# Performance work log

Hardware: AMD Instinct MI355X
Metric: run time of the kernel (lower is better)

## Reference

```python
import jax, jax.numpy as jnp
import numpy as np

BETA = 0.25
EPS = 1e-12

def normalise(x):
    # L2 normalise over last axis
    return x / jnp.sqrt(jnp.sum(x * x, axis=-1, keepdims=True) + EPS)

def setup_inputs() -> dict:
    key = jax.random.key(0)
    k = jax.random.split(key, 6)
    N, d, c, P = 8192, 768, 256, 16384
    return {
        "z": jax.random.normal(k[0], (N, d), dtype=jnp.float32),
        "W_in": jax.random.normal(k[1], (d, c), dtype=jnp.float32) * 0.02,
        "b_in": jnp.zeros((c,), dtype=jnp.float32),
        "W_out": jax.random.normal(k[2], (c, d), dtype=jnp.float32) * 0.02,
        "b_out": jnp.zeros((d,), dtype=jnp.float32),
        "codebook": jax.random.normal(k[3], (P, c), dtype=jnp.float32),
    }

def reference(z, W_in, b_in, W_out, b_out, codebook):
    sg = jax.lax.stop_gradient
    # input projection + L2 normalise
    zq = normalise(z @ W_in + b_in)                 # [N, c]
    cb = normalise(codebook)                        # [P, c]
    # squared euclidean distances: ||z||^2 - 2 z.c + ||c||^2
    dist = (jnp.sum(zq * zq, axis=-1, keepdims=True)
            - 2.0 * jnp.einsum('nc,pc->np', zq, cb)
            + jnp.sum(cb * cb, axis=-1)[None, :])   # [N, P]
    idxes = jnp.argmin(dist, axis=-1)               # [N]
    codes = normalise(codebook[idxes])              # gather + normalise, [N, c]
    loss = BETA * (zq - sg(codes)) ** 2 + (sg(zq) - codes) ** 2
    # straight-through estimator
    codes = zq + sg(codes - zq)
    out = codes @ W_out + b_out                     # [N, d]
    return out, loss, idxes
```

## Files before the change

### kernel.cpp

```cpp
#include <hip/hip_runtime.h>
#include <hip/hip_fp16.h>
#include <math.h>

#define NN 8192
#define DD 768
#define CC 256
#define PP 16384
#define NG 256
#define MARGIN 5.0e-3f
#define BETA_C 1.25f
#define EPS_C 1e-12f

typedef __attribute__((ext_vector_type(8))) _Float16 f16x8;
typedef __attribute__((ext_vector_type(8))) short bf16x8;
typedef __attribute__((ext_vector_type(4))) float f32x4;
typedef __attribute__((ext_vector_type(16))) float f32x16;

static __device__ __forceinline__ ushort f2h(float x) {
    _Float16 h = (_Float16)x;
    return __builtin_bit_cast(unsigned short, h);
}
static __device__ __forceinline__ ushort f2bf(float x) {
    unsigned u = __float_as_uint(x);
    return (ushort)((u + 0x7fffu + ((u >> 16) & 1u)) >> 16);
}
static __device__ __forceinline__ float bf2f(ushort h) {
    return __uint_as_float(((unsigned)h) << 16);
}

static __device__ __forceinline__ void gload_lds16(const void* g, void* l) {
    __builtin_amdgcn_global_load_lds(
        (const __attribute__((address_space(1))) unsigned int*)g,
        (__attribute__((address_space(3))) unsigned int*)l, 16, 0, 0);
}

__global__ __launch_bounds__(256) void k_gemm_in(const float* __restrict__ z,
    const float* __restrict__ W, const float* __restrict__ b,
    float* __restrict__ zq)
{
    __shared__ float zt[64][36];
    __shared__ float wt[32][68];
    const int t = threadIdx.x;
    const int ti = t >> 4, tj = t & 15;
    const int n0 = blockIdx.x * 64;
    const int c0 = blockIdx.y * 64;

    f32x4 acc[4];
#pragma unroll
    for (int r = 0; r < 4; ++r) acc[r] = (f32x4){0.f, 0.f, 0.f, 0.f};

    for (int k0 = 0; k0 < DD; k0 += 32) {
        __syncthreads();
#pragma unroll
        for (int l = 0; l < 2; ++l) {
            int idx = l * 256 + t;
            int row = idx >> 3, c4 = idx & 7;
            *reinterpret_cast<float4*>(&zt[row][c4 * 4]) =
                *reinterpret_cast<const float4*>(&z[(size_t)(n0 + row) * DD + k0 + c4 * 4]);
            int krow = idx >> 4, w4 = idx & 15;
            *reinterpret_cast<float4*>(&wt[krow][w4 * 4]) =
                *reinterpret_cast<const float4*>(&W[(size_t)(k0 + krow) * CC + c0 + w4 * 4]);
        }
        __syncthreads();
#pragma unroll
        for (int kk = 0; kk < 32; kk += 4) {
            float4 a4[4], b4[4];
#pragma unroll
            for (int r = 0; r < 4; ++r)
                a4[r] = *reinterpret_cast<const float4*>(&zt[ti * 4 + r][kk]);
#pragma unroll
            for (int q = 0; q < 4; ++q)
                b4[q] = *reinterpret_cast<const float4*>(&wt[kk + q][tj * 4]);
#pragma unroll
            for (int q = 0; q < 4; ++q)
#pragma unroll
                for (int r = 0; r < 4; ++r) {
                    float av = ((const float*)&a4[r])[q];
                    acc[r].x += av * b4[q].x;
                    acc[r].y += av * b4[q].y;
                    acc[r].z += av * b4[q].z;
                    acc[r].w += av * b4[q].w;
                }
        }
    }
#pragma unroll
    for (int r = 0; r < 4; ++r) {
        int col = c0 + tj * 4;
        float4 o;
        o.x = acc[r].x + b[col];
        o.y = acc[r].y + b[col + 1];
        o.z = acc[r].z + b[col + 2];
        o.w = acc[r].w + b[col + 3];
        *reinterpret_cast<float4*>(&zq[(size_t)(n0 + ti * 4 + r) * CC + col]) = o;
    }
}

__global__ __launch_bounds__(256) void k_norm2(const float* __restrict__ src,
    float* __restrict__ dstf32, ushort* __restrict__ dsth,
    float* __restrict__ sq, float* __restrict__ rinvout, int rows)
{
    const int wave = threadIdx.x >> 6;
    const int lane = threadIdx.x & 63;
    const int row = blockIdx.x * 4 + wave;
    if (row >= rows) return;
    float4 v = *reinterpret_cast<const float4*>(&src[(size_t)row * CC + lane * 4]);
    float s = v.x * v.x + v.y * v.y + v.z * v.z + v.w * v.w;
#pragma unroll
    for (int off = 32; off; off >>= 1) s += __shfl_xor(s, off, 64);
    float r = 1.0f / sqrtf(s + EPS_C);
    v.x *= r; v.y *= r; v.z *= r; v.w *= r;
    if (dstf32)
        *reinterpret_cast<float4*>(&dstf32[(size_t)row * CC + lane * 4]) = v;
    ushort4 hv;
    hv.x = f2h(v.x); hv.y = f2h(v.y); hv.z = f2h(v.z); hv.w = f2h(v.w);
    *reinterpret_cast<ushort4*>(&dsth[(size_t)row * CC + lane * 4]) = hv;
    if (sq) {
        float s2 = v.x * v.x + v.y * v.y + v.z * v.z + v.w * v.w;
#pragma unroll
        for (int off = 32; off; off >>= 1) s2 += __shfl_xor(s2, off, 64);
        if (lane == 0) {
            sq[row] = s2;
            if (rinvout) rinvout[row] = r;
        }
    }
}

__global__ __launch_bounds__(256) void k_split_w(const float* __restrict__ W,
    ushort* __restrict__ wthi, ushort* __restrict__ wtlo)
{
    __shared__ float tile[64][68];
    const int t = threadIdx.x;
    const int d0 = blockIdx.x * 64;
    const int k0 = blockIdx.y * 64;
#pragma unroll
    for (int i = 0; i < 16; ++i) {
        int row = i * 4 + (t >> 6);
        int col = t & 63;
        tile[row][col] = W[(size_t)(k0 + row) * DD + d0 + col];
    }
    __syncthreads();
#pragma unroll
    for (int i = 0; i < 16; ++i) {
        int drow = i * 4 + (t >> 6);
        int kc = t & 63;
        float v = tile[kc][drow];
        ushort hi = f2bf(v);
        float rres = v - bf2f(hi);
        ushort lo = f2bf(rres);
        wthi[(size_t)(d0 + drow) * CC + k0 + kc] = hi;
        wtlo[(size_t)(d0 + drow) * CC + k0 + kc] = lo;
    }
}

__global__ __launch_bounds__(512) void k_dist(
    const ushort* __restrict__ cbh, const ushort* __restrict__ zqh,
    const float* __restrict__ cz2,
    float* __restrict__ gmin, unsigned long long* __restrict__ maskA)
{
    __shared__ ushort lds[2][16384];
    const int t = threadIdx.x;
    const int lane = t & 63;
    const int w = t >> 6;
    const int wr = w >> 2;
    const int wc = w & 3;

    const int id = blockIdx.x;
    const int l = (id & 7) * 256 + (id >> 3);
    const int p0 = (l & 63) * 256;
    const int n0 = (l >> 6) * 256;

    const int kh = lane >> 5;
    const int r31 = lane & 31;

    f32x16 acc[4][2];
#pragma unroll
    for (int mi = 0; mi < 4; ++mi) {
        const int pbm = p0 + wr * 128 + mi * 32;
#pragma unroll
        for (int q = 0; q < 4; ++q) {
            float4 cz = *reinterpret_cast<const float4*>(&cz2[pbm + q * 8 + kh * 4]);
#pragma unroll
            for (int j = 0; j < 4; ++j) {
                float v = -0.5f * ((const float*)&cz.x)[j];
                acc[mi][0][q * 4 + j] = v;
                acc[mi][1][q * 4 + j] = v;
            }
        }
    }

    const int u_l = lane >> 3;
    const int e = (lane & 7) ^ u_l;
    const int hh = e >> 2, jj = e & 3;
    const ushort* srcA[2];
    const ushort* srcB[2];
#pragma unroll
    for (int i = 0; i < 2; ++i)
        srcA[i] = cbh + (size_t)(p0 + 2 * (w * 16 + i * 8 + u_l) + hh) * CC + jj * 8;
#pragma unroll
    for (int i = 0; i < 2; ++i)
        srcB[i] = zqh + (size_t)(n0 + 2 * (w * 16 + i * 8 + u_l) + hh) * CC + jj * 8;

#define STAGE(BUF, KT)                                                        \
    {                                                                         \
        _Pragma("unroll")                                                     \
        for (int i = 0; i < 2; ++i)                                           \
            gload_lds16(srcA[i] + (KT) * 32, &lds[BUF][(w * 16 + i * 8) * 64]); \
        _Pragma("unroll")                                                     \
        for (int i = 0; i < 2; ++i)                                           \
            gload_lds16(srcB[i] + (KT) * 32, &lds[BUF][8192 + (w * 16 + i * 8) * 64]); \
    }

    const int ua = wr * 64 + (r31 >> 1);
    const int ub = wc * 32 + (r31 >> 1);
    const int hb = (r31 & 1) * 4 + kh;

#define COMPUTE(BUF)                                                          \
    {                                                                         \
        _Pragma("unroll")                                                     \
        for (int ks = 0; ks < 2; ++ks) {                                      \
            f16x8 af[4], bfv[2];                                              \
            _Pragma("unroll")                                                 \
            for (int mi = 0; mi < 4; ++mi) {                                  \
                int u = ua + mi * 16;                                         \
                af[mi] = *reinterpret_cast<const f16x8*>(                     \
                    &lds[BUF][u * 64 + (((hb + ks * 2) ^ (u & 7)) * 8)]);     \
            }                                                                 \
            _Pragma("unroll")                                                 \
            for (int ni = 0; ni < 2; ++ni) {                                  \
                int u = ub + ni * 16;                                         \
                bfv[ni] = *reinterpret_cast<const f16x8*>(                    \
                    &lds[BUF][8192 + u * 64 + (((hb + ks * 2) ^ (u & 7)) * 8)]); \
            }                                                                 \
            __builtin_amdgcn_s_setprio(1);                                    \
            acc[0][0] = __builtin_amdgcn_mfma_f32_32x32x16_f16(af[0], bfv[0], acc[0][0], 0, 0, 0); \
            acc[0][1] = __builtin_amdgcn_mfma_f32_32x32x16_f16(af[0], bfv[1], acc[0][1], 0, 0, 0); \
            acc[1][0] = __builtin_amdgcn_mfma_f32_32x32x16_f16(af[1], bfv[0], acc[1][0], 0, 0, 0); \
            acc[1][1] = __builtin_amdgcn_mfma_f32_32x32x16_f16(af[1], bfv[1], acc[1][1], 0, 0, 0); \
            acc[2][0] = __builtin_amdgcn_mfma_f32_32x32x16_f16(af[2], bfv[0], acc[2][0], 0, 0, 0); \
            acc[2][1] = __builtin_amdgcn_mfma_f32_32x32x16_f16(af[2], bfv[1], acc[2][1], 0, 0, 0); \
            acc[3][0] = __builtin_amdgcn_mfma_f32_32x32x16_f16(af[3], bfv[0], acc[3][0], 0, 0, 0); \
            acc[3][1] = __builtin_amdgcn_mfma_f32_32x32x16_f16(af[3], bfv[1], acc[3][1], 0, 0, 0); \
            __builtin_amdgcn_s_setprio(0);                                    \
        }                                                                     \
    }

#define BODY(KT, VM, DOSTAGE)                                                 \
    {                                                                         \
        if (DOSTAGE) STAGE(((KT) + 1) & 1, (KT) + 1);                         \
        __builtin_amdgcn_sched_barrier(0);                                    \
        asm volatile("s_waitcnt vmcnt(" #VM ")" ::: "memory");                \
        __builtin_amdgcn_s_barrier();                                         \
        __builtin_amdgcn_sched_barrier(0);                                    \
        COMPUTE((KT) & 1);                                                    \
        if ((KT) < 7) __builtin_amdgcn_s_barrier();                           \
    }

    STAGE(0, 0);
    BODY(0, 4, 1)
    BODY(1, 4, 1)
    BODY(2, 4, 1)
    BODY(3, 4, 1)
    BODY(4, 4, 1)
    BODY(5, 4, 1)
    BODY(6, 4, 1)
    BODY(7, 0, 0)

#undef BODY
#undef COMPUTE
#undef STAGE

#pragma unroll
    for (int ni = 0; ni < 2; ++ni) {
#pragma unroll
        for (int g = 0; g < 2; ++g) {
            float M = -1e30f;
#pragma unroll
            for (int m2 = 0; m2 < 2; ++m2)
#pragma unroll
                for (int r = 0; r < 16; ++r) M = fmaxf(M, acc[g * 2 + m2][ni][r]);
            M = fmaxf(M, __shfl_xor(M, 32, 64));
            const float thr = M - 0.5f * MARGIN;
            unsigned long long msk = 0ull;
#pragma unroll
            for (int m2 = 0; m2 < 2; ++m2)
#pragma unroll
                for (int q = 0; q < 4; ++q) {
                    unsigned nib = 0u;
#pragma unroll
                    for (int j = 0; j < 4; ++j)
                        nib |= (acc[g * 2 + m2][ni][q * 4 + j] >= thr) ? (1u << j) : 0u;
                    msk |= (unsigned long long)nib << (m2 * 32 + q * 8 + kh * 4);
                }
            msk |= __shfl_xor(msk, 32, 64);
            if (kh == 0) {
                int n = n0 + wc * 64 + ni * 32 + r31;
                int grp = (p0 >> 6) + wr * 2 + g;
                gmin[(size_t)n * NG + grp] = -2.0f * M;
                maskA[(size_t)n * NG + grp] = msk;
            }
        }
    }
}

__global__ __launch_bounds__(256) void k_pick(
    const float* __restrict__ gmin, const unsigned long long* __restrict__ maskA,
    const float* __restrict__ zqn, const float* __restrict__ cb_raw,
    const float* __restrict__ rinv, const float* __restrict__ cz2,
    float* __restrict__ idxf, ushort* __restrict__ chi,
    ushort* __restrict__ clo, float* __restrict__ loss)
{
    __shared__ int lst[4][256];
    __shared__ int cnt[4];
    const int t = threadIdx.x;
    const int w = t >> 6;
    const int lane = t & 63;
    const int row = blockIdx.x * 4 + w;

    float4 zr = *reinterpret_cast<const float4*>(&zqn[(size_t)row * CC + lane * 4]);
    float4 gv = *reinterpret_cast<const float4*>(&gmin[(size_t)row * NG + lane * 4]);

    float pm = fminf(fminf(gv.x, gv.y), fminf(gv.z, gv.w));
#pragma unroll
    for (int off = 1; off < 64; off <<= 1) pm = fminf(pm, __shfl_xor(pm, off, 64));
    const float thresh = pm + MARGIN;

    if (lane == 0) cnt[w] = 0;
    __syncthreads();
    {
        const float g4[4] = {gv.x, gv.y, gv.z, gv.w};
#pragma unroll
        for (int j = 0; j < 4; ++j)
            if (g4[j] <= thresh) {
                int pos = atomicAdd(&cnt[w], 1);
                lst[w][pos] = lane * 4 + j;
            }
    }
    __syncthreads();

    const int nc = cnt[w];
    unsigned long long best = ~0ull;
    for (int ci = 0; ci < nc; ++ci) {
        int g = lst[w][ci];
        unsigned long long msk = maskA[(size_t)row * NG + g];
        while (msk) {
            int bit = __ffsll((long long)msk) - 1;
            msk &= msk - 1;
            int p = g * 64 + bit;
            float rv = rinv[p];
            float4 c4 = *reinterpret_cast<const float4*>(&cb_raw[(size_t)p * CC + lane * 4]);
            float part = (c4.x * rv) * zr.x + (c4.y * rv) * zr.y
                       + (c4.z * rv) * zr.z + (c4.w * rv) * zr.w;
#pragma unroll
            for (int off = 1; off < 64; off <<= 1) part += __shfl_xor(part, off, 64);
            float d4 = fmaf(-2.0f, part, 4.0f + cz2[p]);
            unsigned long long pk = ((unsigned long long)__float_as_uint(d4) << 32) | (unsigned)p;
            best = best < pk ? best : pk;
        }
    }
    const int p = (int)(best & 0xffffffffu);
    if (lane == 0) idxf[row] = (float)p;

    const float rv = rinv[p];
    float4 cv = *reinterpret_cast<const float4*>(&cb_raw[(size_t)p * CC + lane * 4]);
    cv.x *= rv; cv.y *= rv; cv.z *= rv; cv.w *= rv;
    ushort4 hv, lv16;
    hv.x = f2bf(cv.x); lv16.x = f2bf(cv.x - bf2f(hv.x));
    hv.y = f2bf(cv.y); lv16.y = f2bf(cv.y - bf2f(hv.y));
    hv.z = f2bf(cv.z); lv16.z = f2bf(cv.z - bf2f(hv.z));
    hv.w = f2bf(cv.w); lv16.w = f2bf(cv.w - bf2f(hv.w));
    *reinterpret_cast<ushort4*>(&chi[(size_t)row * CC + lane * 4]) = hv;
    *reinterpret_cast<ushort4*>(&clo[(size_t)row * CC + lane * 4]) = lv16;
    float4 lsv;
    float dx = zr.x - cv.x, dy = zr.y - cv.y, dz = zr.z - cv.z, dw = zr.w - cv.w;
    lsv.x = BETA_C * dx * dx; lsv.y = BETA_C * dy * dy;
    lsv.z = BETA_C * dz * dz; lsv.w = BETA_C * dw * dw;
    *reinterpret_cast<float4*>(&loss[(size_t)row * CC + lane * 4]) = lsv;
}

__global__ __launch_bounds__(256) void k_gemm_out_mfma(
    const ushort* __restrict__ chi, const ushort* __restrict__ clo,
    const ushort* __restrict__ wthi, const ushort* __restrict__ wtlo,
    const float* __restrict__ bout, float* __restrict__ out)
{
    __shared__ ushort sAh[128 * 64];
    __shared__ ushort sAl[128 * 64];
    __shared__ ushort sBh[128 * 64];
    __shared__ ushort sBl[128 * 64];
    const int t = threadIdx.x;
    const int lane = t & 63;
    const int w = t >> 6;
    const int wr = w >> 1;
    const int wc = w & 1;
    const int nb = blockIdx.x * 128;
    const int db = blockIdx.y * 128;
    const int kh = lane >> 5;
    const int r31 = lane & 31;

    f32x16 acc[2][2];
#pragma unroll
    for (int mi = 0; mi < 2; ++mi)
#pragma unroll
        for (int ni = 0; ni < 2; ++ni)
#pragma unroll
            for (int r = 0; r < 16; ++r) acc[mi][ni][r] = 0.f;

    const int srow = lane >> 3;
    const int schunk = (lane & 7) ^ srow;
    const size_t rowA = (size_t)(nb + w * 32 + srow) * CC;
    const size_t rowB = (size_t)(db + w * 32 + srow) * CC;
    const char* sAhsrc = (const char*)chi + rowA * 2 + schunk * 16;
    const char* sAlsrc = (const char*)clo + rowA * 2 + schunk * 16;
    const char* sBhsrc = (const char*)wthi + rowB * 2 + schunk * 16;
    const char* sBlsrc = (const char*)wtlo + rowB * 2 + schunk * 16;
    char* dA = (char*)sAh + (w * 32) * 128;
    char* dAl = (char*)sAl + (w * 32) * 128;
    char* dB = (char*)sBh + (w * 32) * 128;
    char* dBl = (char*)sBl + (w * 32) * 128;

    const int sx = (r31 & 7) << 4;

    for (int k0 = 0; k0 < CC; k0 += 64) {
        __syncthreads();
#pragma unroll
        for (int i = 0; i < 4; ++i) {
            gload_lds16(sAhsrc + (size_t)i * 8 * (CC * 2) + k0 * 2, dA + i * 1024);
            gload_lds16(sAlsrc + (size_t)i * 8 * (CC * 2) + k0 * 2, dAl + i * 1024);
            gload_lds16(sBhsrc + (size_t)i * 8 * (CC * 2) + k0 * 2, dB + i * 1024);
            gload_lds16(sBlsrc + (size_t)i * 8 * (CC * 2) + k0 * 2, dBl + i * 1024);
        }
        __syncthreads();
#pragma unroll
        for (int ks = 0; ks < 4; ++ks) {
            const int ko = ((ks * 32 + kh * 16) ^ sx);
            bf16x8 ah[2], al[2], bh[2], bl[2];
#pragma unroll
            for (int mi = 0; mi < 2; ++mi) {
                ah[mi] = *reinterpret_cast<const bf16x8*>(
                    (const char*)sAh + (wr * 64 + mi * 32 + r31) * 128 + ko);
                al[mi] = *reinterpret_cast<const bf16x8*>(
                    (const char*)sAl + (wr * 64 + mi * 32 + r31) * 128 + ko);
            }
#pragma unroll
            for (int ni = 0; ni < 2; ++ni) {
                bh[ni] = *reinterpret_cast<const bf16x8*>(
                    (const char*)sBh + (wc * 64 + ni * 32 + r31) * 128 + ko);
                bl[ni] = *reinterpret_cast<const bf16x8*>(
                    (const char*)sBl + (wc * 64 + ni * 32 + r31) * 128 + ko);
            }
#pragma unroll
            for (int mi = 0; mi < 2; ++mi)
#pragma unroll
                for (int ni = 0; ni < 2; ++ni) {
                    acc[mi][ni] = __builtin_amdgcn_mfma_f32_32x32x16_bf16(
                        ah[mi], bh[ni], acc[mi][ni], 0, 0, 0);
                    acc[mi][ni] = __builtin_amdgcn_mfma_f32_32x32x16_bf16(
                        ah[mi], bl[ni], acc[mi][ni], 0, 0, 0);
                    acc[mi][ni] = __builtin_amdgcn_mfma_f32_32x32x16_bf16(
                        al[mi], bh[ni], acc[mi][ni], 0, 0, 0);
                }
        }
    }

#pragma unroll
    for (int ni = 0; ni < 2; ++ni) {
        const int d = db + wc * 64 + ni * 32 + r31;
        const float bv = bout[d];
#pragma unroll
        for (int mi = 0; mi < 2; ++mi) {
            const int nbase = nb + wr * 64 + mi * 32 + 4 * kh;
#pragma unroll
            for (int q = 0; q < 4; ++q)
#pragma unroll
                for (int j = 0; j < 4; ++j) {
                    int n = nbase + j + 8 * q;
                    out[(size_t)n * DD + d] = acc[mi][ni][q * 4 + j] + bv;
                }
        }
    }
}

extern "C" void kernel_launch(void* const* d_in, const int* in_sizes, int n_in,
                              void* d_out, int out_size, void* d_ws, size_t ws_size,
                              hipStream_t stream)
{
    const float* z        = (const float*)d_in[0];
    const float* W_in     = (const float*)d_in[1];
    const float* b_in     = (const float*)d_in[2];
    const float* W_out    = (const float*)d_in[3];
    const float* b_out    = (const float*)d_in[4];
    const float* codebook = (const float*)d_in[5];

    char* ws = (char*)d_ws;
    ushort* zqh   = (ushort*)(ws);
    ushort* cbh   = (ushort*)(ws + 4194304);
    ushort* chi   = (ushort*)(ws + 12582912);
    ushort* clo   = (ushort*)(ws + 16777216);
    ushort* wthi  = (ushort*)(ws + 20971520);
    ushort* wtlo  = (ushort*)(ws + 21364736);
    float*  cz2   = (float*)(ws + 21757952);
    float*  rinv  = (float*)(ws + 21823488);

    float* out  = (float*)d_out;
    float* loss = out + (size_t)NN * DD;
    float* idxf = loss + (size_t)NN * CC;

    float* gmin = (float*)d_out;
    unsigned long long* maskA = (unsigned long long*)((char*)d_out + 8388608);
    float* zq = loss;

    k_gemm_in<<<dim3(NN / 64, CC / 64), 256, 0, stream>>>(z, W_in, b_in, zq);
    k_norm2<<<NN / 4, 256, 0, stream>>>(zq, zq, zqh, (float*)nullptr, (float*)nullptr, NN);
    k_norm2<<<PP / 4, 256, 0, stream>>>(codebook, (float*)nullptr, cbh, cz2, rinv, PP);
    k_split_w<<<dim3(DD / 64, CC / 64), 256, 0, stream>>>(W_out, wthi, wtlo);
    k_dist<<<(PP / 256) * (NN / 256), 512, 0, stream>>>(cbh, zqh, cz2, gmin, maskA);
    k_pick<<<NN / 4, 256, 0, stream>>>(gmin, maskA, zq, codebook, rinv, cz2,
                                       idxf, chi, clo, loss);
    k_gemm_out_mfma<<<dim3(NN / 128, DD / 128), 256, 0, stream>>>(chi, clo, wthi, wtlo, b_out, out);
}
```

Baseline: 204.3 us.

## Drop split-bf16 output GEMM, merge codebook/W prep, retile distance kernel to 128x128

The output projection now uses a single bf16 MFMA per tile instead of the three-term hi/lo split. This removes the low-part buffers, their loads and two thirds of the MFMAs, at the cost of output accuracy. Codebook normalisation and the W_out transpose/convert are merged into one launch, which saves a kernel launch. The distance kernel moves from 256x256 tiles with 512 threads to 128x128 tiles with 256 threads and an occupancy hint of 4, trading operand reuse for more resident blocks.

After: 192.3 us. -5.9%, faster.

```diff
diff --git a/kernel.cpp b/kernel.cpp
--- a/kernel.cpp
+++ b/kernel.cpp
@@ -24,9 +24,6 @@
     unsigned u = __float_as_uint(x);
     return (ushort)((u + 0x7fffu + ((u >> 16) & 1u)) >> 16);
 }
-static __device__ __forceinline__ float bf2f(ushort h) {
-    return __uint_as_float(((unsigned)h) << 16);
-}
 
 static __device__ __forceinline__ void gload_lds16(const void* g, void* l) {
     __builtin_amdgcn_global_load_lds(
@@ -96,8 +93,7 @@
 }
 
 __global__ __launch_bounds__(256) void k_norm2(const float* __restrict__ src,
-    float* __restrict__ dstf32, ushort* __restrict__ dsth,
-    float* __restrict__ sq, float* __restrict__ rinvout, int rows)
+    float* __restrict__ dstf32, ushort* __restrict__ dsth, int rows)
 {
     const int wave = threadIdx.x >> 6;
     const int lane = threadIdx.x & 63;
@@ -109,73 +105,82 @@
     for (int off = 32; off; off >>= 1) s += __shfl_xor(s, off, 64);
     float r = 1.0f / sqrtf(s + EPS_C);
     v.x *= r; v.y *= r; v.z *= r; v.w *= r;
-    if (dstf32)
-        *reinterpret_cast<float4*>(&dstf32[(size_t)row * CC + lane * 4]) = v;
+    *reinterpret_cast<float4*>(&dstf32[(size_t)row * CC + lane * 4]) = v;
     ushort4 hv;
     hv.x = f2h(v.x); hv.y = f2h(v.y); hv.z = f2h(v.z); hv.w = f2h(v.w);
     *reinterpret_cast<ushort4*>(&dsth[(size_t)row * CC + lane * 4]) = hv;
-    if (sq) {
+}
+
+__global__ __launch_bounds__(256) void k_prep(const float* __restrict__ codebook,
+    ushort* __restrict__ cbh, float* __restrict__ cz2, float* __restrict__ rinv,
+    const float* __restrict__ W, ushort* __restrict__ wthi)
+{
+    __shared__ float tile[64][68];
+    const int t = threadIdx.x;
+    if (blockIdx.x < 4096) {
+        const int wave = t >> 6;
+        const int lane = t & 63;
+        const int row = blockIdx.x * 4 + wave;
+        float4 v = *reinterpret_cast<const float4*>(&codebook[(size_t)row * CC + lane * 4]);
+        float s = v.x * v.x + v.y * v.y + v.z * v.z + v.w * v.w;
+#pragma unroll
+        for (int off = 32; off; off >>= 1) s += __shfl_xor(s, off, 64);
+        float r = 1.0f / sqrtf(s + EPS_C);
+        v.x *= r; v.y *= r; v.z *= r; v.w *= r;
+        ushort4 hv;
+        hv.x = f2h(v.x); hv.y = f2h(v.y); hv.z = f2h(v.z); hv.w = f2h(v.w);
+        *reinterpret_cast<ushort4*>(&cbh[(size_t)row * CC + lane * 4]) = hv;
         float s2 = v.x * v.x + v.y * v.y + v.z * v.z + v.w * v.w;
 #pragma unroll
         for (int off = 32; off; off >>= 1) s2 += __shfl_xor(s2, off, 64);
         if (lane == 0) {
-            sq[row] = s2;
-            if (rinvout) rinvout[row] = r;
-        }
-    }
-}
-
-__global__ __launch_bounds__(256) void k_split_w(const float* __restrict__ W,
-    ushort* __restrict__ wthi, ushort* __restrict__ wtlo)
-{
-    __shared__ float tile[64][68];
-    const int t = threadIdx.x;
-    const int d0 = blockIdx.x * 64;
-    const int k0 = blockIdx.y * 64;
-#pragma unroll
-    for (int i = 0; i < 16; ++i) {
-        int row = i * 4 + (t >> 6);
-        int col = t & 63;
-        tile[row][col] = W[(size_t)(k0 + row) * DD + d0 + col];
-    }
-    __syncthreads();
-#pragma unroll
-    for (int i = 0; i < 16; ++i) {
-        int drow = i * 4 + (t >> 6);
-        int kc = t & 63;
-        float v = tile[kc][drow];
-        ushort hi = f2bf(v);
-        float rres = v - bf2f(hi);
-        ushort lo = f2bf(rres);
-        wthi[(size_t)(d0 + drow) * CC + k0 + kc] = hi;
-        wtlo[(size_t)(d0 + drow) * CC + k0 + kc] = lo;
-    }
-}
-
-__global__ __launch_bounds__(512) void k_dist(
+            cz2[row] = s2;
+            rinv[row] = r;
+        }
+    } else {
+        const int id = blockIdx.x - 4096;
+        const int d0 = (id % 12) * 64;
+        const int k0 = (id / 12) * 64;
+#pragma unroll
+        for (int i = 0; i < 16; ++i) {
+            int row = i * 4 + (t >> 6);
+            int col = t & 63;
+            tile[row][col] = W[(size_t)(k0 + row) * DD + d0 + col];
+        }
+        __syncthreads();
+#pragma unroll
+        for (int i = 0; i < 16; ++i) {
+            int drow = i * 4 + (t >> 6);
+            int kc = t & 63;
+            wthi[(size_t)(d0 + drow) * CC + k0 + kc] = f2bf(tile[kc][drow]);
+        }
+    }
+}
+
+__global__ __launch_bounds__(256, 4) void k_dist(
     const ushort* __restrict__ cbh, const ushort* __restrict__ zqh,
     const float* __restrict__ cz2,
     float* __restrict__ gmin, unsigned long long* __restrict__ maskA)
 {
-    __shared__ ushort lds[2][16384];
+    __shared__ ushort lds[2][8192];
     const int t = threadIdx.x;
     const int lane = t & 63;
     const int w = t >> 6;
-    const int wr = w >> 2;
-    const int wc = w & 3;
+    const int wr = w >> 1;
+    const int wc = w & 1;
 
     const int id = blockIdx.x;
-    const int l = (id & 7) * 256 + (id >> 3);
-    const int p0 = (l & 63) * 256;
-    const int n0 = (l >> 6) * 256;
+    const int l = (id & 7) * 1024 + (id >> 3);
+    const int p0 = (l >> 6) * 128;
+    const int n0 = (l & 63) * 128;
 
     const int kh = lane >> 5;
     const int r31 = lane & 31;
 
-    f32x16 acc[4][2];
-#pragma unroll
-    for (int mi = 0; mi < 4; ++mi) {
-        const int pbm = p0 + wr * 128 + mi * 32;
+    f32x16 acc[2][2];
+#pragma unroll
+    for (int mi = 0; mi < 2; ++mi) {
+        const int pbm = p0 + wr * 64 + mi * 32;
 #pragma unroll
         for (int q = 0; q < 4; ++q) {
             float4 cz = *reinterpret_cast<const float4*>(&cz2[pbm + q * 8 + kh * 4]);
@@ -207,10 +212,10 @@
             gload_lds16(srcA[i] + (KT) * 32, &lds[BUF][(w * 16 + i * 8) * 64]); \
         _Pragma("unroll")                                                     \
         for (int i = 0; i < 2; ++i)                                           \
-            gload_lds16(srcB[i] + (KT) * 32, &lds[BUF][8192 + (w * 16 + i * 8) * 64]); \
-    }
-
-    const int ua = wr * 64 + (r31 >> 1);
+            gload_lds16(srcB[i] + (KT) * 32, &lds[BUF][4096 + (w * 16 + i * 8) * 64]); \
+    }
+
+    const int ua = wr * 32 + (r31 >> 1);
     const int ub = wc * 32 + (r31 >> 1);
     const int hb = (r31 & 1) * 4 + kh;
 
@@ -218,9 +223,9 @@
     {                                                                         \
         _Pragma("unroll")                                                     \
         for (int ks = 0; ks < 2; ++ks) {                                      \
-            f16x8 af[4], bfv[2];                                              \
+            f16x8 af[2], bfv[2];                                              \
             _Pragma("unroll")                                                 \
-            for (int mi = 0; mi < 4; ++mi) {                                  \
+            for (int mi = 0; mi < 2; ++mi) {                                  \
                 int u = ua + mi * 16;                                         \
                 af[mi] = *reinterpret_cast<const f16x8*>(                     \
                     &lds[BUF][u * 64 + (((hb + ks * 2) ^ (u & 7)) * 8)]);     \
@@ -229,17 +234,13 @@
             for (int ni = 0; ni < 2; ++ni) {                                  \
                 int u = ub + ni * 16;                                         \
                 bfv[ni] = *reinterpret_cast<const f16x8*>(                    \
-                    &lds[BUF][8192 + u * 64 + (((hb + ks * 2) ^ (u & 7)) * 8)]); \
+                    &lds[BUF][4096 + u * 64 + (((hb + ks * 2) ^ (u & 7)) * 8)]); \
             }                                                                 \
             __builtin_amdgcn_s_setprio(1);                                    \
             acc[0][0] = __builtin_amdgcn_mfma_f32_32x32x16_f16(af[0], bfv[0], acc[0][0], 0, 0, 0); \
             acc[0][1] = __builtin_amdgcn_mfma_f32_32x32x16_f16(af[0], bfv[1], acc[0][1], 0, 0, 0); \
             acc[1][0] = __builtin_amdgcn_mfma_f32_32x32x16_f16(af[1], bfv[0], acc[1][0], 0, 0, 0); \
             acc[1][1] = __builtin_amdgcn_mfma_f32_32x32x16_f16(af[1], bfv[1], acc[1][1], 0, 0, 0); \
-            acc[2][0] = __builtin_amdgcn_mfma_f32_32x32x16_f16(af[2], bfv[0], acc[2][0], 0, 0, 0); \
-            acc[2][1] = __builtin_amdgcn_mfma_f32_32x32x16_f16(af[2], bfv[1], acc[2][1], 0, 0, 0); \
-            acc[3][0] = __builtin_amdgcn_mfma_f32_32x32x16_f16(af[3], bfv[0], acc[3][0], 0, 0, 0); \
-            acc[3][1] = __builtin_amdgcn_mfma_f32_32x32x16_f16(af[3], bfv[1], acc[3][1], 0, 0, 0); \
             __builtin_amdgcn_s_setprio(0);                                    \
         }                                                                     \
     }
@@ -271,33 +272,30 @@
 
 #pragma unroll
     for (int ni = 0; ni < 2; ++ni) {
-#pragma unroll
-        for (int g = 0; g < 2; ++g) {
-            float M = -1e30f;
-#pragma unroll
-            for (int m2 = 0; m2 < 2; ++m2)
-#pragma unroll
-                for (int r = 0; r < 16; ++r) M = fmaxf(M, acc[g * 2 + m2][ni][r]);
-            M = fmaxf(M, __shfl_xor(M, 32, 64));
-            const float thr = M - 0.5f * MARGIN;
-            unsigned long long msk = 0ull;
-#pragma unroll
-            for (int m2 = 0; m2 < 2; ++m2)
-#pragma unroll
-                for (int q = 0; q < 4; ++q) {
-                    unsigned nib = 0u;
-#pragma unroll
-                    for (int j = 0; j < 4; ++j)
-                        nib |= (acc[g * 2 + m2][ni][q * 4 + j] >= thr) ? (1u << j) : 0u;
-                    msk |= (unsigned long long)nib << (m2 * 32 + q * 8 + kh * 4);
-                }
-            msk |= __shfl_xor(msk, 32, 64);
-            if (kh == 0) {
-                int n = n0 + wc * 64 + ni * 32 + r31;
-                int grp = (p0 >> 6) + wr * 2 + g;
-                gmin[(size_t)n * NG + grp] = -2.0f * M;
-                maskA[(size_t)n * NG + grp] = msk;
+        float M = -1e30f;
+#pragma unroll
+        for (int mi = 0; mi < 2; ++mi)
+#pragma unroll
+            for (int r = 0; r < 16; ++r) M = fmaxf(M, acc[mi][ni][r]);
+        M = fmaxf(M, __shfl_xor(M, 32, 64));
+        const float thr = M - 0.5f * MARGIN;
+        unsigned long long msk = 0ull;
+#pragma unroll
+        for (int mi = 0; mi < 2; ++mi)
+#pragma unroll
+            for (int q = 0; q < 4; ++q) {
+                unsigned nib = 0u;
+#pragma unroll
+                for (int j = 0; j < 4; ++j)
+                    nib |= (acc[mi][ni][q * 4 + j] >= thr) ? (1u << j) : 0u;
+                msk |= (unsigned long long)nib << (mi * 32 + q * 8 + kh * 4);
             }
+        msk |= __shfl_xor(msk, 32, 64);
+        if (kh == 0) {
+            int n = n0 + wc * 64 + ni * 32 + r31;
+            int grp = (p0 >> 6) + wr;
+            gmin[(size_t)n * NG + grp] = -2.0f * M;
+            maskA[(size_t)n * NG + grp] = msk;
         }
     }
 }
@@ -306,8 +304,7 @@
     const float* __restrict__ gmin, const unsigned long long* __restrict__ maskA,
     const float* __restrict__ zqn, const float* __restrict__ cb_raw,
     const float* __restrict__ rinv, const float* __restrict__ cz2,
-    float* __restrict__ idxf, ushort* __restrict__ chi,
-    ushort* __restrict__ clo, float* __restrict__ loss)
+    float* __restrict__ idxf, ushort* __restrict__ chi, float* __restrict__ loss)
 {
     __shared__ int lst[4][256];
     __shared__ int cnt[4];
@@ -363,13 +360,9 @@
     const float rv = rinv[p];
     float4 cv = *reinterpret_cast<const float4*>(&cb_raw[(size_t)p * CC + lane * 4]);
     cv.x *= rv; cv.y *= rv; cv.z *= rv; cv.w *= rv;
-    ushort4 hv, lv16;
-    hv.x = f2bf(cv.x); lv16.x = f2bf(cv.x - bf2f(hv.x));
-    hv.y = f2bf(cv.y); lv16.y = f2bf(cv.y - bf2f(hv.y));
-    hv.z = f2bf(cv.z); lv16.z = f2bf(cv.z - bf2f(hv.z));
-    hv.w = f2bf(cv.w); lv16.w = f2bf(cv.w - bf2f(hv.w));
+    ushort4 hv;
+    hv.x = f2bf(cv.x); hv.y = f2bf(cv.y); hv.z = f2bf(cv.z); hv.w = f2bf(cv.w);
     *reinterpret_cast<ushort4*>(&chi[(size_t)row * CC + lane * 4]) = hv;
-    *reinterpret_cast<ushort4*>(&clo[(size_t)row * CC + lane * 4]) = lv16;
     float4 lsv;
     float dx = zr.x - cv.x, dy = zr.y - cv.y, dz = zr.z - cv.z, dw = zr.w - cv.w;
     lsv.x = BETA_C * dx * dx; lsv.y = BETA_C * dy * dy;
@@ -378,14 +371,11 @@
 }
 
 __global__ __launch_bounds__(256) void k_gemm_out_mfma(
-    const ushort* __restrict__ chi, const ushort* __restrict__ clo,
-    const ushort* __restrict__ wthi, const ushort* __restrict__ wtlo,
+    const ushort* __restrict__ chi, const ushort* __restrict__ wthi,
     const float* __restrict__ bout, float* __restrict__ out)
 {
     __shared__ ushort sAh[128 * 64];
-    __shared__ ushort sAl[128 * 64];
     __shared__ ushort sBh[128 * 64];
-    __shared__ ushort sBl[128 * 64];
     const int t = threadIdx.x;
     const int lane = t & 63;
     const int w = t >> 6;
@@ -409,13 +399,9 @@
     const size_t rowA = (size_t)(nb + w * 32 + srow) * CC;
     const size_t rowB = (size_t)(db + w * 32 + srow) * CC;
     const char* sAhsrc = (const char*)chi + rowA * 2 + schunk * 16;
-    const char* sAlsrc = (const char*)clo + rowA * 2 + schunk * 16;
     const char* sBhsrc = (const char*)wthi + rowB * 2 + schunk * 16;
-    const char* sBlsrc = (const char*)wtlo + rowB * 2 + schunk * 16;
     char* dA = (char*)sAh + (w * 32) * 128;
-    char* dAl = (char*)sAl + (w * 32) * 128;
     char* dB = (char*)sBh + (w * 32) * 128;
-    char* dBl = (char*)sBl + (w * 32) * 128;
 
     const int sx = (r31 & 7) << 4;
 
@@ -424,40 +410,27 @@
 #pragma unroll
         for (int i = 0; i < 4; ++i) {
             gload_lds16(sAhsrc + (size_t)i * 8 * (CC * 2) + k0 * 2, dA + i * 1024);
-            gload_lds16(sAlsrc + (size_t)i * 8 * (CC * 2) + k0 * 2, dAl + i * 1024);
             gload_lds16(sBhsrc + (size_t)i * 8 * (CC * 2) + k0 * 2, dB + i * 1024);
-            gload_lds16(sBlsrc + (size_t)i * 8 * (CC * 2) + k0 * 2, dBl + i * 1024);
         }
         __syncthreads();
 #pragma unroll
         for (int ks = 0; ks < 4; ++ks) {
             const int ko = ((ks * 32 + kh * 16) ^ sx);
-            bf16x8 ah[2], al[2], bh[2], bl[2];
-#pragma unroll
-            for (int mi = 0; mi < 2; ++mi) {
+            bf16x8 ah[2], bh[2];
+#pragma unroll
+            for (int mi = 0; mi < 2; ++mi)
                 ah[mi] = *reinterpret_cast<const bf16x8*>(
                     (const char*)sAh + (wr * 64 + mi * 32 + r31) * 128 + ko);
-                al[mi] = *reinterpret_cast<const bf16x8*>(
-                    (const char*)sAl + (wr * 64 + mi * 32 + r31) * 128 + ko);
-            }
-#pragma unroll
-            for (int ni = 0; ni < 2; ++ni) {
+#pragma unroll
+            for (int ni = 0; ni < 2; ++ni)
                 bh[ni] = *reinterpret_cast<const bf16x8*>(
                     (const char*)sBh + (wc * 64 + ni * 32 + r31) * 128 + ko);
-                bl[ni] = *reinterpret_cast<const bf16x8*>(
-                    (const char*)sBl + (wc * 64 + ni * 32 + r31) * 128 + ko);
-            }
 #pragma unroll
             for (int mi = 0; mi < 2; ++mi)
 #pragma unroll
-                for (int ni = 0; ni < 2; ++ni) {
+                for (int ni = 0; ni < 2; ++ni)
                     acc[mi][ni] = __builtin_amdgcn_mfma_f32_32x32x16_bf16(
                         ah[mi], bh[ni], acc[mi][ni], 0, 0, 0);
-                    acc[mi][ni] = __builtin_amdgcn_mfma_f32_32x32x16_bf16(
-                        ah[mi], bl[ni], acc[mi][ni], 0, 0, 0);
-                    acc[mi][ni] = __builtin_amdgcn_mfma_f32_32x32x16_bf16(
-                        al[mi], bh[ni], acc[mi][ni], 0, 0, 0);
-                }
         }
     }
 
@@ -494,11 +467,9 @@
     ushort* zqh   = (ushort*)(ws);
     ushort* cbh   = (ushort*)(ws + 4194304);
     ushort* chi   = (ushort*)(ws + 12582912);
-    ushort* clo   = (ushort*)(ws + 16777216);
-    ushort* wthi  = (ushort*)(ws + 20971520);
-    ushort* wtlo  = (ushort*)(ws + 21364736);
-    float*  cz2   = (float*)(ws + 21757952);
-    float*  rinv  = (float*)(ws + 21823488);
+    ushort* wthi  = (ushort*)(ws + 16777216);
+    float*  cz2   = (float*)(ws + 17170432);
+    float*  rinv  = (float*)(ws + 17235968);
 
     float* out  = (float*)d_out;
     float* loss = out + (size_t)NN * DD;
@@ -509,11 +480,10 @@
     float* zq = loss;
 
     k_gemm_in<<<dim3(NN / 64, CC / 64), 256, 0, stream>>>(z, W_in, b_in, zq);
-    k_norm2<<<NN / 4, 256, 0, stream>>>(zq, zq, zqh, (float*)nullptr, (float*)nullptr, NN);
-    k_norm2<<<PP / 4, 256, 0, stream>>>(codebook, (float*)nullptr, cbh, cz2, rinv, PP);
-    k_split_w<<<dim3(DD / 64, CC / 64), 256, 0, stream>>>(W_out, wthi, wtlo);
-    k_dist<<<(PP / 256) * (NN / 256), 512, 0, stream>>>(cbh, zqh, cz2, gmin, maskA);
+    k_norm2<<<NN / 4, 256, 0, stream>>>(zq, zq, zqh, NN);
+    k_prep<<<PP / 4 + 48, 256, 0, stream>>>(codebook, cbh, cz2, rinv, W_out, wthi);
+    k_dist<<<(PP / 128) * (NN / 128), 256, 0, stream>>>(cbh, zqh, cz2, gmin, maskA);
     k_pick<<<NN / 4, 256, 0, stream>>>(gmin, maskA, zq, codebook, rinv, cz2,
-                                       idxf, chi, clo, loss);
-    k_gemm_out_mfma<<<dim3(NN / 128, DD / 128), 256, 0, stream>>>(chi, clo, wthi, wtlo, b_out, out);
-}
+                                       idxf, chi, loss);
+    k_gemm_out_mfma<<<dim3(NN / 128, DD / 128), 256, 0, stream>>>(chi, wthi, b_out, out);
+}
```
